# Kernel tuning notes

Measured on AMD Instinct MI355X. Metric: run time of the kernel, lower is better.

The kernel has to match this reference:

```python
import jax, jax.numpy as jnp
import numpy as np

N = 4096          # N_TARGET_NODES (node count == feature dim)
E = 262144        # number of directed edges (avg degree 64)


def setup_inputs() -> dict:
    key = jax.random.key(0)
    k1, k2, k3, k4 = jax.random.split(key, 4)
    x = jax.random.normal(k1, (N, N), dtype=jnp.float32)
    edge_index = jax.random.randint(k2, (2, E), 0, N, dtype=jnp.int32)
    # scale weights so sigmoid inputs are O(1)
    W1 = jax.random.normal(k3, (N, N), dtype=jnp.float32) * (1.0 / np.sqrt(N))
    b1 = jnp.zeros((N,), dtype=jnp.float32)
    W2 = jax.random.normal(k4, (N, 1), dtype=jnp.float32) * (1.0 / np.sqrt(N))
    b2 = jnp.zeros((1,), dtype=jnp.float32)
    return {"x": x, "edge_index": edge_index, "W1": W1, "b1": b1, "W2": W2, "b2": b2}


def _gcn_conv(x, edge_index, W, b):
    """PyG GCNConv: h = D^{-1/2}(A+I)D^{-1/2} (x W) + b, edge weights = 1."""
    n = x.shape[0]
    h = x @ W                                   # [n, out]
    loop = jnp.arange(n, dtype=edge_index.dtype)
    src = jnp.concatenate([edge_index[0], loop])  # add self loops
    dst = jnp.concatenate([edge_index[1], loop])
    deg = jax.ops.segment_sum(jnp.ones_like(src, dtype=h.dtype), dst, num_segments=n)
    dinv = jnp.where(deg > 0, jax.lax.rsqrt(deg), 0.0)
    norm = dinv[src] * dinv[dst]                # [E+n]
    msg = h[src] * norm[:, None]                # gather + scale
    out = jax.ops.segment_sum(msg, dst, num_segments=n)  # scatter-add at targets
    return out + b


def reference(x, edge_index, W1, b1, W2, b2):
    # torch.squeeze(x) is a no-op for 2-D x
    x1 = jax.nn.sigmoid(_gcn_conv(x, edge_index, W1, b1))
    # F.dropout in eval mode is identity (deterministic reference)
    x2 = jax.nn.sigmoid(_gcn_conv(x1, edge_index, W2, b2))
    return x2  # [N, 1]
```

## Files before the change

### kernel.cpp

```cpp
#include <hip/hip_runtime.h>


typedef __attribute__((ext_vector_type(8))) short bf16x8;
typedef __attribute__((ext_vector_type(4))) float f32x4;

#define NN 4096
#define NT 64

__device__ __forceinline__ unsigned f2bf(float f) {
  unsigned u = __float_as_uint(f);
  return (u + 0x7FFFu + ((u >> 16) & 1u)) >> 16;
}

#define GLDS(g, l) __builtin_amdgcn_global_load_lds(                      \
    (const __attribute__((address_space(1))) void*)(g),                   \
    (__attribute__((address_space(3))) void*)(l), 16, 0, 0)


__global__ void init_deg_kernel(float* deg) {
  int v = blockIdx.x * 256 + threadIdx.x;
  if (v < NN) deg[v] = 1.0f;
}

__global__ void count_deg_kernel(const int* __restrict__ dst, int E, float* deg) {
  int e = blockIdx.x * 256 + threadIdx.x;
  if (e < E) atomicAdd(&deg[dst[e]], 1.0f);
}

__global__ void dinv_kernel(const float* __restrict__ deg, float* __restrict__ dinv) {
  int v = blockIdx.x * 256 + threadIdx.x;
  if (v < NN) dinv[v] = rsqrtf(deg[v]);
}

__global__ void diag_kernel(const float* __restrict__ dinv, float* __restrict__ S) {
  int v = blockIdx.x * 256 + threadIdx.x;
  if (v < NN) { float d = dinv[v]; S[(size_t)v * NN + v] = d * d; }
}

__global__ void scatter_S_kernel(const int* __restrict__ src, const int* __restrict__ dst,
                                 int E, const float* __restrict__ dinv, float* __restrict__ S) {
  int e = blockIdx.x * 256 + threadIdx.x;
  if (e < E) {
    int s = src[e], d = dst[e];
    atomicAdd(&S[(size_t)d * NN + s], dinv[s] * dinv[d]);
  }
}


__global__ void cast_kernel(const float* __restrict__ in, unsigned short* __restrict__ out, int n) {
  int i = (blockIdx.x * 256 + threadIdx.x) * 8;
  if (i >= n) return;
  const float4* p = (const float4*)(in + i);
  float4 a = p[0], b = p[1];
  uint4 o;
  o.x = f2bf(a.x) | (f2bf(a.y) << 16);
  o.y = f2bf(a.z) | (f2bf(a.w) << 16);
  o.z = f2bf(b.x) | (f2bf(b.y) << 16);
  o.w = f2bf(b.z) | (f2bf(b.w) << 16);
  *(uint4*)(out + i) = o;
}

__global__ void transpose_cast_kernel(const float* __restrict__ W, unsigned short* __restrict__ WT) {
  __shared__ float tile[32][33];
  int bx = blockIdx.x * 32, by = blockIdx.y * 32;
  int tx = threadIdx.x, ty = threadIdx.y;
#pragma unroll
  for (int i = 0; i < 32; i += 8)
    tile[ty + i][tx] = W[(size_t)(by + ty + i) * NN + bx + tx];
  __syncthreads();
#pragma unroll
  for (int i = 0; i < 32; i += 8)
    WT[(size_t)(bx + ty + i) * NN + by + tx] = (unsigned short)f2bf(tile[tx][ty + i]);
}


template <int EPI>
__global__ __launch_bounds__(512, 2) void gemm256_kernel(
    const unsigned short* __restrict__ A, const unsigned short* __restrict__ BT,
    unsigned short* __restrict__ C, const float* __restrict__ bias) {
  __shared__ __align__(16) char smem[131072];
  const int tid = threadIdx.x;
  const int lane = tid & 63, wid = tid >> 6;
  const int wr = wid >> 2, wc = wid & 3;

  const int bid = blockIdx.x;
  const int swz = (bid & 7) * 32 + (bid >> 3);
  const int rowBase = (swz >> 4) * 256;
  const int colBase = (swz & 15) * 256;

  const int srow = tid >> 3;
  const int scolb = ((tid & 7) << 4) ^ ((srow & 7) << 4);
  const unsigned short* pA = A + (size_t)(rowBase + srow) * NN + (scolb >> 1);
  const unsigned short* pB = BT + (size_t)(colBase + srow) * NN + (scolb >> 1);

  const int rl = lane & 15;
  const int c0 = ((lane >> 4) << 4) ^ ((lane & 7) << 4);
  const int c1 = c0 ^ 64;
  const int aoff = (wr * 128 + rl) * 128;
  const int boff = 32768 + (wc * 64 + rl) * 128;

  f32x4 acc[8][4] = {};

  {
    char* w0 = smem + (wid << 10);
    char* w1 = smem + 65536 + (wid << 10);
    GLDS(pB + (size_t)0 * 64 * NN, w0 + 32768 + 0 * 8192);
    GLDS(pB + (size_t)1 * 64 * NN, w0 + 32768 + 1 * 8192);
    GLDS(pB + (size_t)2 * 64 * NN, w0 + 32768 + 2 * 8192);
    GLDS(pB + (size_t)3 * 64 * NN, w0 + 32768 + 3 * 8192);
    GLDS(pA + (size_t)0 * 64 * NN, w0 + 0 * 8192);
    GLDS(pA + (size_t)2 * 64 * NN, w0 + 2 * 8192);
    GLDS(pA + (size_t)1 * 64 * NN, w0 + 1 * 8192);
    GLDS(pA + (size_t)3 * 64 * NN, w0 + 3 * 8192);
    GLDS(pA + 64 + (size_t)0 * 64 * NN, w1 + 0 * 8192);
    GLDS(pA + 64 + (size_t)2 * 64 * NN, w1 + 2 * 8192);
    asm volatile("s_waitcnt vmcnt(2)" ::: "memory");
    __builtin_amdgcn_s_barrier();
  }

  for (int t = 0; t < NT; ++t) {
    const int cur = (t & 1) << 16;
    const char* lb = smem + cur;
    char* stN = smem + (cur ^ 65536) + (wid << 10);
    char* stC = smem + cur + (wid << 10);
    const unsigned short* s1A = pA + ((t + 1) & 63) * 64;
    const unsigned short* s1B = pB + ((t + 1) & 63) * 64;
    const unsigned short* s2A = pA + ((t + 2) & 63) * 64;

    bf16x8 af[4], bk0[4], bk1[4];

#pragma unroll
    for (int m = 0; m < 4; ++m) af[m] = *(const bf16x8*)(lb + aoff + m * 2048 + c0);
#pragma unroll
    for (int n = 0; n < 4; ++n) bk0[n] = *(const bf16x8*)(lb + boff + n * 2048 + c0);
    GLDS(s1B + (size_t)0 * 64 * NN, stN + 32768 + 0 * 8192);
    GLDS(s1B + (size_t)1 * 64 * NN, stN + 32768 + 1 * 8192);
    __builtin_amdgcn_s_barrier();
    asm volatile("s_waitcnt lgkmcnt(0)" ::: "memory");
    __builtin_amdgcn_sched_barrier(0);
    __builtin_amdgcn_s_setprio(1);
#pragma unroll
    for (int m = 0; m < 4; ++m)
#pragma unroll
      for (int n = 0; n < 4; ++n)
        acc[m][n] = __builtin_amdgcn_mfma_f32_16x16x32_bf16(af[m], bk0[n], acc[m][n], 0, 0, 0);
    __builtin_amdgcn_s_setprio(0);
    __builtin_amdgcn_s_barrier();

#pragma unroll
    for (int m = 0; m < 4; ++m) af[m] = *(const bf16x8*)(lb + aoff + m * 2048 + c1);
#pragma unroll
    for (int n = 0; n < 4; ++n) bk1[n] = *(const bf16x8*)(lb + boff + n * 2048 + c1);
    GLDS(s1B + (size_t)2 * 64 * NN, stN + 32768 + 2 * 8192);
    GLDS(s1B + (size_t)3 * 64 * NN, stN + 32768 + 3 * 8192);
    __builtin_amdgcn_s_barrier();
    asm volatile("s_waitcnt lgkmcnt(0)" ::: "memory");
    __builtin_amdgcn_sched_barrier(0);
    __builtin_amdgcn_s_setprio(1);
#pragma unroll
    for (int m = 0; m < 4; ++m)
#pragma unroll
      for (int n = 0; n < 4; ++n)
        acc[m][n] = __builtin_amdgcn_mfma_f32_16x16x32_bf16(af[m], bk1[n], acc[m][n], 0, 0, 0);
    __builtin_amdgcn_s_setprio(0);
    asm volatile("s_waitcnt vmcnt(6)" ::: "memory");
    __builtin_amdgcn_s_barrier();

#pragma unroll
    for (int m = 0; m < 4; ++m) af[m] = *(const bf16x8*)(lb + aoff + (4 + m) * 2048 + c0);
    GLDS(s1A + (size_t)1 * 64 * NN, stN + 1 * 8192);
    GLDS(s1A + (size_t)3 * 64 * NN, stN + 3 * 8192);
    __builtin_amdgcn_s_barrier();
    asm volatile("s_waitcnt lgkmcnt(0)" ::: "memory");
    __builtin_amdgcn_sched_barrier(0);
    __builtin_amdgcn_s_setprio(1);
#pragma unroll
    for (int m = 0; m < 4; ++m)
#pragma unroll
      for (int n = 0; n < 4; ++n)
        acc[4 + m][n] = __builtin_amdgcn_mfma_f32_16x16x32_bf16(af[m], bk0[n], acc[4 + m][n], 0, 0, 0);
    __builtin_amdgcn_s_setprio(0);
    __builtin_amdgcn_s_barrier();

#pragma unroll
    for (int m = 0; m < 4; ++m) af[m] = *(const bf16x8*)(lb + aoff + (4 + m) * 2048 + c1);
    GLDS(s2A + (size_t)0 * 64 * NN, stC + 0 * 8192);
    GLDS(s2A + (size_t)2 * 64 * NN, stC + 2 * 8192);
    __builtin_amdgcn_s_barrier();
    asm volatile("s_waitcnt lgkmcnt(0)" ::: "memory");
    __builtin_amdgcn_sched_barrier(0);
    __builtin_amdgcn_s_setprio(1);
#pragma unroll
    for (int m = 0; m < 4; ++m)
#pragma unroll
      for (int n = 0; n < 4; ++n)
        acc[4 + m][n] = __builtin_amdgcn_mfma_f32_16x16x32_bf16(af[m], bk1[n], acc[4 + m][n], 0, 0, 0);
    __builtin_amdgcn_s_setprio(0);
    asm volatile("s_waitcnt vmcnt(4)" ::: "memory");
    __builtin_amdgcn_s_barrier();
  }

  const int orow = rowBase + wr * 128 + (lane >> 4) * 4;
  const int ocol = colBase + wc * 64 + (lane & 15);
#pragma unroll
  for (int n = 0; n < 4; ++n) {
    int ccol = ocol + n * 16;
    float bv = (EPI == 1) ? bias[ccol] : 0.0f;
#pragma unroll
    for (int m = 0; m < 8; ++m) {
#pragma unroll
      for (int i = 0; i < 4; ++i) {
        float x = acc[m][n][i] + bv;
        if (EPI == 1) x = 1.0f / (1.0f + __expf(-x));
        C[(size_t)(orow + m * 16 + i) * NN + ccol] = (unsigned short)f2bf(x);
      }
    }
  }
}


__global__ void matvec_kernel(const unsigned short* __restrict__ X1,
                              const float* __restrict__ W2, float* __restrict__ h2) {
  int row = blockIdx.x, t = threadIdx.x;
  const unsigned short* xr = X1 + (size_t)row * NN;
  float s = 0.0f;
  for (int j = t * 8; j < NN; j += 2048) {
    uint4 u = *(const uint4*)(xr + j);
    unsigned v[4] = {u.x, u.y, u.z, u.w};
#pragma unroll
    for (int q = 0; q < 4; ++q) {
      float lo = __uint_as_float(v[q] << 16);
      float hi = __uint_as_float(v[q] & 0xFFFF0000u);
      s += lo * W2[j + q * 2] + hi * W2[j + q * 2 + 1];
    }
  }
#pragma unroll
  for (int off = 32; off > 0; off >>= 1) s += __shfl_down(s, off);
  __shared__ float wsum[4];
  if ((t & 63) == 0) wsum[t >> 6] = s;
  __syncthreads();
  if (t == 0) h2[row] = wsum[0] + wsum[1] + wsum[2] + wsum[3];
}

__global__ void init_t_kernel(const float* __restrict__ dinv, const float* __restrict__ h2,
                              const float* __restrict__ b2, float* __restrict__ tacc) {
  int v = blockIdx.x * 256 + threadIdx.x;
  if (v < NN) tacc[v] = dinv[v] * dinv[v] * h2[v] + b2[0];
}

__global__ void scatter_t_kernel(const int* __restrict__ src, const int* __restrict__ dst,
                                 int E, const float* __restrict__ dinv,
                                 const float* __restrict__ h2, float* __restrict__ tacc) {
  int e = blockIdx.x * 256 + threadIdx.x;
  if (e < E) {
    int s = src[e], d = dst[e];
    atomicAdd(&tacc[d], dinv[s] * dinv[d] * h2[s]);
  }
}

__global__ void final_kernel(const float* __restrict__ tacc, float* __restrict__ out) {
  int v = blockIdx.x * 256 + threadIdx.x;
  if (v < NN) out[v] = 1.0f / (1.0f + __expf(-tacc[v]));
}


extern "C" void kernel_launch(void* const* d_in, const int* in_sizes, int n_in,
                              void* d_out, int out_size, void* d_ws, size_t ws_size,
                              hipStream_t stream) {
  const float* x  = (const float*)d_in[0];
  const int*   ei = (const int*)d_in[1];
  const float* W1 = (const float*)d_in[2];
  const float* b1 = (const float*)d_in[3];
  const float* W2 = (const float*)d_in[4];
  const float* b2 = (const float*)d_in[5];
  float* out = (float*)d_out;
  const int E = in_sizes[1] / 2;
  const int* esrc = ei;
  const int* edst = ei + E;

  char* w = (char*)d_ws;
  float*          Sf  = (float*)w;
  unsigned short* H1T = (unsigned short*)w;
  unsigned short* W1T = (unsigned short*)(w + (size_t)(32u << 20));
  unsigned short* Sbf = (unsigned short*)(w + (size_t)(64u << 20));
  unsigned short* Xbf = (unsigned short*)(w + (size_t)(96u << 20));
  float* deg  = (float*)(w + (size_t)(128u << 20));
  float* dinv = deg + 4096;
  float* h2   = deg + 8192;
  float* tacc = deg + 12288;

  init_deg_kernel<<<16, 256, 0, stream>>>(deg);
  count_deg_kernel<<<(E + 255) / 256, 256, 0, stream>>>(edst, E, deg);
  dinv_kernel<<<16, 256, 0, stream>>>(deg, dinv);

  hipMemsetAsync(Sf, 0, (size_t)64 << 20, stream);
  diag_kernel<<<16, 256, 0, stream>>>(dinv, Sf);
  scatter_S_kernel<<<(E + 255) / 256, 256, 0, stream>>>(esrc, edst, E, dinv, Sf);
  cast_kernel<<<8192, 256, 0, stream>>>(Sf, Sbf, NN * NN);

  cast_kernel<<<8192, 256, 0, stream>>>(x, Xbf, NN * NN);
  transpose_cast_kernel<<<dim3(128, 128), dim3(32, 8), 0, stream>>>(W1, W1T);

  gemm256_kernel<0><<<256, 512, 0, stream>>>(W1T, Xbf, H1T, nullptr);
  gemm256_kernel<1><<<256, 512, 0, stream>>>(Sbf, H1T, Xbf, b1);

  matvec_kernel<<<4096, 256, 0, stream>>>(Xbf, W2, h2);
  init_t_kernel<<<16, 256, 0, stream>>>(dinv, h2, b2, tacc);
  scatter_t_kernel<<<(E + 255) / 256, 256, 0, stream>>>(esrc, edst, E, dinv, h2, tacc);
  final_kernel<<<16, 256, 0, stream>>>(tacc, out);
}
```

Before: 367.0 us.

## Restructure GEMM main loop to one barrier per K-step with register prefetch

Rewrites the bf16 GEMM main loop from four barrier-separated phases to a single barrier per K-tile. LDS fragment reads for the next sub-step are issued while the current MFMA block runs, and the next tile's first fragments are preloaded after the barrier. The cross-tile A prefetch into the current buffer is dropped, and the loop is unrolled by two. This aims to cut synchronisation stalls and hide LDS latency, at the cost of more live registers and tighter reliance on correct vmcnt accounting.

```diff
diff --git a/kernel.cpp b/kernel.cpp
--- a/kernel.cpp
+++ b/kernel.cpp
@@ -100,10 +100,10 @@
   const int boff = 32768 + (wc * 64 + rl) * 128;
 
   f32x4 acc[8][4] = {};
+  bf16x8 bk0[4], bk1[4], afA[4], afB[4];
 
   {
     char* w0 = smem + (wid << 10);
-    char* w1 = smem + 65536 + (wid << 10);
     GLDS(pB + (size_t)0 * 64 * NN, w0 + 32768 + 0 * 8192);
     GLDS(pB + (size_t)1 * 64 * NN, w0 + 32768 + 1 * 8192);
     GLDS(pB + (size_t)2 * 64 * NN, w0 + 32768 + 2 * 8192);
@@ -112,92 +112,83 @@
     GLDS(pA + (size_t)2 * 64 * NN, w0 + 2 * 8192);
     GLDS(pA + (size_t)1 * 64 * NN, w0 + 1 * 8192);
     GLDS(pA + (size_t)3 * 64 * NN, w0 + 3 * 8192);
-    GLDS(pA + 64 + (size_t)0 * 64 * NN, w1 + 0 * 8192);
-    GLDS(pA + 64 + (size_t)2 * 64 * NN, w1 + 2 * 8192);
     asm volatile("s_waitcnt vmcnt(2)" ::: "memory");
     __builtin_amdgcn_s_barrier();
-  }
-
+#pragma unroll
+    for (int m = 0; m < 4; ++m) afA[m] = *(const bf16x8*)(smem + aoff + m * 2048 + c0);
+#pragma unroll
+    for (int n = 0; n < 4; ++n) bk0[n] = *(const bf16x8*)(smem + boff + n * 2048 + c0);
+  }
+
+#pragma unroll 2
   for (int t = 0; t < NT; ++t) {
-    const int cur = (t & 1) << 16;
-    const char* lb = smem + cur;
-    char* stN = smem + (cur ^ 65536) + (wid << 10);
-    char* stC = smem + cur + (wid << 10);
+    const char* lb = smem + ((t & 1) << 16);
+    char* st = smem + (((t & 1) ^ 1) << 16) + (wid << 10);
     const unsigned short* s1A = pA + ((t + 1) & 63) * 64;
     const unsigned short* s1B = pB + ((t + 1) & 63) * 64;
-    const unsigned short* s2A = pA + ((t + 2) & 63) * 64;
-
-    bf16x8 af[4], bk0[4], bk1[4];
-
-#pragma unroll
-    for (int m = 0; m < 4; ++m) af[m] = *(const bf16x8*)(lb + aoff + m * 2048 + c0);
-#pragma unroll
-    for (int n = 0; n < 4; ++n) bk0[n] = *(const bf16x8*)(lb + boff + n * 2048 + c0);
-    GLDS(s1B + (size_t)0 * 64 * NN, stN + 32768 + 0 * 8192);
-    GLDS(s1B + (size_t)1 * 64 * NN, stN + 32768 + 1 * 8192);
+
+    GLDS(s1B + (size_t)0 * 64 * NN, st + 32768 + 0 * 8192);
+    GLDS(s1B + (size_t)1 * 64 * NN, st + 32768 + 1 * 8192);
+    GLDS(s1B + (size_t)2 * 64 * NN, st + 32768 + 2 * 8192);
+#pragma unroll
+    for (int m = 0; m < 4; ++m) afB[m] = *(const bf16x8*)(lb + aoff + m * 2048 + c1);
+#pragma unroll
+    for (int n = 0; n < 4; ++n) bk1[n] = *(const bf16x8*)(lb + boff + n * 2048 + c1);
+    __builtin_amdgcn_s_setprio(1);
+#pragma unroll
+    for (int m = 0; m < 4; ++m)
+#pragma unroll
+      for (int n = 0; n < 4; ++n)
+        acc[m][n] = __builtin_amdgcn_mfma_f32_16x16x32_bf16(afA[m], bk0[n], acc[m][n], 0, 0, 0);
+    __builtin_amdgcn_s_setprio(0);
+    asm volatile("s_waitcnt vmcnt(3)" ::: "memory");
+    __builtin_amdgcn_sched_barrier(0);
+
+    GLDS(s1B + (size_t)3 * 64 * NN, st + 32768 + 3 * 8192);
+    GLDS(s1A + (size_t)0 * 64 * NN, st + 0 * 8192);
+    GLDS(s1A + (size_t)2 * 64 * NN, st + 2 * 8192);
+#pragma unroll
+    for (int m = 0; m < 4; ++m) afA[m] = *(const bf16x8*)(lb + aoff + (4 + m) * 2048 + c0);
+    __builtin_amdgcn_s_setprio(1);
+#pragma unroll
+    for (int m = 0; m < 4; ++m)
+#pragma unroll
+      for (int n = 0; n < 4; ++n)
+        acc[m][n] = __builtin_amdgcn_mfma_f32_16x16x32_bf16(afB[m], bk1[n], acc[m][n], 0, 0, 0);
+    __builtin_amdgcn_s_setprio(0);
+    __builtin_amdgcn_sched_barrier(0);
+
+    GLDS(s1A + (size_t)1 * 64 * NN, st + 1 * 8192);
+    GLDS(s1A + (size_t)3 * 64 * NN, st + 3 * 8192);
+#pragma unroll
+    for (int m = 0; m < 4; ++m) afB[m] = *(const bf16x8*)(lb + aoff + (4 + m) * 2048 + c1);
+    __builtin_amdgcn_s_setprio(1);
+#pragma unroll
+    for (int m = 0; m < 4; ++m)
+#pragma unroll
+      for (int n = 0; n < 4; ++n)
+        acc[4 + m][n] = __builtin_amdgcn_mfma_f32_16x16x32_bf16(afA[m], bk0[n], acc[4 + m][n], 0, 0, 0);
+    __builtin_amdgcn_s_setprio(0);
+    __builtin_amdgcn_sched_barrier(0);
+
+    __builtin_amdgcn_s_setprio(1);
+#pragma unroll
+    for (int m = 0; m < 4; ++m)
+#pragma unroll
+      for (int n = 0; n < 4; ++n)
+        acc[4 + m][n] = __builtin_amdgcn_mfma_f32_16x16x32_bf16(afB[m], bk1[n], acc[4 + m][n], 0, 0, 0);
+    __builtin_amdgcn_s_setprio(0);
+    asm volatile("s_waitcnt lgkmcnt(0)" ::: "memory");
+    asm volatile("s_waitcnt vmcnt(2)" ::: "memory");
     __builtin_amdgcn_s_barrier();
-    asm volatile("s_waitcnt lgkmcnt(0)" ::: "memory");
+    {
+      const char* nb = smem + (((t + 1) & 1) << 16);
+#pragma unroll
+      for (int m = 0; m < 4; ++m) afA[m] = *(const bf16x8*)(nb + aoff + m * 2048 + c0);
+#pragma unroll
+      for (int n = 0; n < 4; ++n) bk0[n] = *(const bf16x8*)(nb + boff + n * 2048 + c0);
+    }
     __builtin_amdgcn_sched_barrier(0);
-    __builtin_amdgcn_s_setprio(1);
-#pragma unroll
-    for (int m = 0; m < 4; ++m)
-#pragma unroll
-      for (int n = 0; n < 4; ++n)
-        acc[m][n] = __builtin_amdgcn_mfma_f32_16x16x32_bf16(af[m], bk0[n], acc[m][n], 0, 0, 0);
-    __builtin_amdgcn_s_setprio(0);
-    __builtin_amdgcn_s_barrier();
-
-#pragma unroll
-    for (int m = 0; m < 4; ++m) af[m] = *(const bf16x8*)(lb + aoff + m * 2048 + c1);
-#pragma unroll
-    for (int n = 0; n < 4; ++n) bk1[n] = *(const bf16x8*)(lb + boff + n * 2048 + c1);
-    GLDS(s1B + (size_t)2 * 64 * NN, stN + 32768 + 2 * 8192);
-    GLDS(s1B + (size_t)3 * 64 * NN, stN + 32768 + 3 * 8192);
-    __builtin_amdgcn_s_barrier();
-    asm volatile("s_waitcnt lgkmcnt(0)" ::: "memory");
-    __builtin_amdgcn_sched_barrier(0);
-    __builtin_amdgcn_s_setprio(1);
-#pragma unroll
-    for (int m = 0; m < 4; ++m)
-#pragma unroll
-      for (int n = 0; n < 4; ++n)
-        acc[m][n] = __builtin_amdgcn_mfma_f32_16x16x32_bf16(af[m], bk1[n], acc[m][n], 0, 0, 0);
-    __builtin_amdgcn_s_setprio(0);
-    asm volatile("s_waitcnt vmcnt(6)" ::: "memory");
-    __builtin_amdgcn_s_barrier();
-
-#pragma unroll
-    for (int m = 0; m < 4; ++m) af[m] = *(const bf16x8*)(lb + aoff + (4 + m) * 2048 + c0);
-    GLDS(s1A + (size_t)1 * 64 * NN, stN + 1 * 8192);
-    GLDS(s1A + (size_t)3 * 64 * NN, stN + 3 * 8192);
-    __builtin_amdgcn_s_barrier();
-    asm volatile("s_waitcnt lgkmcnt(0)" ::: "memory");
-    __builtin_amdgcn_sched_barrier(0);
-    __builtin_amdgcn_s_setprio(1);
-#pragma unroll
-    for (int m = 0; m < 4; ++m)
-#pragma unroll
-      for (int n = 0; n < 4; ++n)
-        acc[4 + m][n] = __builtin_amdgcn_mfma_f32_16x16x32_bf16(af[m], bk0[n], acc[4 + m][n], 0, 0, 0);
-    __builtin_amdgcn_s_setprio(0);
-    __builtin_amdgcn_s_barrier();
-
-#pragma unroll
-    for (int m = 0; m < 4; ++m) af[m] = *(const bf16x8*)(lb + aoff + (4 + m) * 2048 + c1);
-    GLDS(s2A + (size_t)0 * 64 * NN, stC + 0 * 8192);
-    GLDS(s2A + (size_t)2 * 64 * NN, stC + 2 * 8192);
-    __builtin_amdgcn_s_barrier();
-    asm volatile("s_waitcnt lgkmcnt(0)" ::: "memory");
-    __builtin_amdgcn_sched_barrier(0);
-    __builtin_amdgcn_s_setprio(1);
-#pragma unroll
-    for (int m = 0; m < 4; ++m)
-#pragma unroll
-      for (int n = 0; n < 4; ++n)
-        acc[4 + m][n] = __builtin_amdgcn_mfma_f32_16x16x32_bf16(af[m], bk1[n], acc[4 + m][n], 0, 0, 0);
-    __builtin_amdgcn_s_setprio(0);
-    asm volatile("s_waitcnt vmcnt(4)" ::: "memory");
-    __builtin_amdgcn_s_barrier();
   }
 
   const int orow = rowBase + wr * 128 + (lane >> 4) * 4;
```

After: 353.6 us. 1.04x faster.
